# Kernel optimization log

Measured on AMD Instinct MI355X. Metric: run time of the kernel, lower is better.

Reference implementation:

```python
import jax, jax.numpy as jnp
import numpy as np

KH, KW = 3, 3
STRIDE, PAD, DIL = 1, 1, 1
GROUPS, DG = 1, 1
B, C, H, W = 4, 64, 96, 96
O = 64
K = KH * KW


def setup_inputs() -> dict:
    key = jax.random.key(0)
    k1, k2, k3, k4 = jax.random.split(key, 4)
    x = jax.random.normal(k1, (B, C, H, W), dtype=jnp.float32)
    offset = jax.random.normal(k2, (B, DG * 2 * K, H, W), dtype=jnp.float32)
    mask = jax.random.uniform(k3, (B, DG * K, H, W), dtype=jnp.float32)
    stdv = 1.0 / np.sqrt(C * KH * KW)
    weight = jax.random.uniform(k4, (O, C // GROUPS, KH, KW), dtype=jnp.float32,
                                minval=-stdv, maxval=stdv)
    bias = jnp.zeros((O,), dtype=jnp.float32)
    return {"x": x, "offset": offset, "mask": mask, "weight": weight, "bias": bias}


def _dcn(x, offset, mask, weight, bias):
    Bc, Cc, Hc, Wc = x.shape
    Ho = (Hc + 2 * PAD - DIL * (KH - 1) - 1) // STRIDE + 1
    Wo = (Wc + 2 * PAD - DIL * (KW - 1) - 1) // STRIDE + 1
    Cg = Cc // DG
    dt = x.dtype

    # offset channels per deform group: [k, (y,x)] interleaved (mmcv layout)
    off = offset.reshape(Bc, DG, K, 2, Ho, Wo)
    off_y, off_x = off[:, :, :, 0], off[:, :, :, 1]          # [B,DG,K,Ho,Wo]
    m = mask.reshape(Bc, DG, K, Ho, Wo)

    ky = (jnp.arange(K) // KW).astype(dt) * DIL               # kernel tap dy
    kx = (jnp.arange(K) % KW).astype(dt) * DIL                # kernel tap dx
    base_y = (jnp.arange(Ho) * STRIDE - PAD).astype(dt)
    base_x = (jnp.arange(Wo) * STRIDE - PAD).astype(dt)
    py = base_y[None, None, None, :, None] + ky[None, None, :, None, None] + off_y
    px = base_x[None, None, None, None, :] + kx[None, None, :, None, None] + off_x

    y0 = jnp.floor(py)
    x0 = jnp.floor(px)
    ly = py - y0
    lx = px - x0
    y0i = y0.astype(jnp.int32)
    x0i = x0.astype(jnp.int32)

    x_flat = x.reshape(Bc, DG, Cg, Hc * Wc)

    def gather(yi, xi):
        # zero-padding semantics: out-of-range corners contribute 0
        valid = ((yi >= 0) & (yi < Hc) & (xi >= 0) & (xi < Wc)).astype(dt)
        idx = jnp.clip(yi, 0, Hc - 1) * Wc + jnp.clip(xi, 0, Wc - 1)
        idx_b = jnp.broadcast_to(idx.reshape(Bc, DG, 1, K * Ho * Wo),
                                 (Bc, DG, Cg, K * Ho * Wo))
        vals = jnp.take_along_axis(x_flat, idx_b, axis=3)
        return vals.reshape(Bc, DG, Cg, K, Ho, Wo), valid

    v00, m00 = gather(y0i, x0i)
    v01, m01 = gather(y0i, x0i + 1)
    v10, m10 = gather(y0i + 1, x0i)
    v11, m11 = gather(y0i + 1, x0i + 1)

    w00 = ((1 - ly) * (1 - lx) * m00)[:, :, None]             # [B,DG,1,K,Ho,Wo]
    w01 = ((1 - ly) * lx * m01)[:, :, None]
    w10 = (ly * (1 - lx) * m10)[:, :, None]
    w11 = (ly * lx * m11)[:, :, None]

    sampled = v00 * w00 + v01 * w01 + v10 * w10 + v11 * w11   # bilinear
    sampled = sampled * m[:, :, None]                         # mask modulation
    s = sampled.reshape(Bc, Cc, K, Ho, Wo)

    out = jnp.einsum('ock,bckhw->bohw', weight.reshape(O, Cc, K), s)
    return out + bias[None, :, None, None]


def reference(x, offset, mask, weight, bias):
    return _dcn(x, offset, mask, weight, bias)
```

## Files before the change

### kernel.cpp

```cpp
#include <hip/hip_runtime.h>

#define Bn 4
#define Cn 64
#define Hn 96
#define Wn 96
#define On 64
#define Kn 9
#define HWn (Hn*Wn)
#define NT 256
#define TP 16
#define TW (Wn/TP)
#define NBLK (Bn*Hn*TW)
#define SSTRIDE 584
#define NWELEM (18*4*64*8)

typedef __attribute__((ext_vector_type(8))) short bf16x8;
typedef __attribute__((ext_vector_type(4))) short bf16x4;
typedef __attribute__((ext_vector_type(4))) float f32x4;

__device__ __forceinline__ unsigned short f2bf(float f) {
    unsigned u = __float_as_uint(f);
    u += 0x7FFFu + ((u >> 16) & 1u);
    return (unsigned short)(u >> 16);
}
__device__ __forceinline__ float bf2f(unsigned short h) {
    return __uint_as_float((unsigned)h << 16);
}
__device__ __forceinline__ unsigned cvtpk(float a, float b) {
    return (unsigned)f2bf(a) | ((unsigned)f2bf(b) << 16);
}

__global__ __launch_bounds__(NT) void prep_kernel(
    const float* __restrict__ x, const float* __restrict__ w,
    unsigned short* __restrict__ xT, unsigned short* __restrict__ wbfA)
{
    __shared__ unsigned short tile[Cn * Wn];
    const int tid = threadIdx.x;
    if (blockIdx.x < Bn * Hn) {
        const int b = blockIdx.x / Hn;
        const int h = blockIdx.x - b * Hn;
        #pragma unroll
        for (int i = 0; i < (Cn * Wn) / NT; ++i) {
            int e = i * NT + tid;
            int c = e / Wn, ww = e - c * Wn;
            tile[c * Wn + ww] = f2bf(x[(((size_t)b * Cn + c) * Hn + h) * Wn + ww]);
        }
        __syncthreads();
        #pragma unroll
        for (int i = 0; i < (Wn * 8) / NT; ++i) {
            int s = i * NT + tid;
            int ww = s >> 3, g = s & 7;
            unsigned short hh[8];
            #pragma unroll
            for (int j = 0; j < 8; ++j) hh[j] = tile[(g * 8 + j) * Wn + ww];
            uint4 pk;
            pk.x = hh[0] | ((unsigned)hh[1] << 16);
            pk.y = hh[2] | ((unsigned)hh[3] << 16);
            pk.z = hh[4] | ((unsigned)hh[5] << 16);
            pk.w = hh[6] | ((unsigned)hh[7] << 16);
            *(uint4*)&xT[(((size_t)b * Hn + h) * Wn + ww) * Cn + g * 8] = pk;
        }
    } else {
        int i = (blockIdx.x - Bn * Hn) * NT + tid;
        if (i < NWELEM) {
            int j  = i & 7;
            int l  = (i >> 3) & 63;
            int wv = (i >> 9) & 3;
            int t  = i >> 11;
            int o  = wv * 16 + (l & 15);
            int kp = t * 32 + (l >> 4) * 8 + j;
            wbfA[i] = f2bf(w[(o * Cn + (kp & 63)) * Kn + (kp >> 6)]);
        }
    }
}

__global__ __launch_bounds__(NT, 4) void dcn5_kernel(
    const unsigned short* __restrict__ xT, const float* __restrict__ offset,
    const float* __restrict__ mask, const float* __restrict__ bias,
    const unsigned short* __restrict__ wbfA, float* __restrict__ out)
{
    __shared__ float4 lwv[4][36];
    __shared__ int4   liv[4][36];
    __shared__ __align__(16) unsigned short Slds[TP * SSTRIDE];

    const int tid  = threadIdx.x;
    const int wave = tid >> 6;
    const int lane = tid & 63;

    const int p = blockIdx.x;
    const int v = (p & 7) * (NBLK / 8) + (p >> 3);
    const int b  = v / (Hn * TW);
    int rem      = v - b * (Hn * TW);
    const int ho = rem / TW;
    const int wt = rem - ho * TW;
    const int wo0 = wt * TP;

    const bf16x8* Af = (const bf16x8*)wbfA;
    bf16x8 aReg[3];
    aReg[0] = Af[(0 * 4 + wave) * 64 + lane];
    aReg[1] = Af[(1 * 4 + wave) * 64 + lane];
    aReg[2] = Af[(2 * 4 + wave) * 64 + lane];

    if (lane < 36) {
        int k  = lane >> 2;
        int pl = lane & 3;
        int wo = wo0 + wave * 4 + pl;
        float oy = offset[((b * (2*Kn) + 2*k    ) * Hn + ho) * Wn + wo];
        float ox = offset[((b * (2*Kn) + 2*k + 1) * Hn + ho) * Wn + wo];
        float mm = mask  [((b * Kn + k) * Hn + ho) * Wn + wo];
        float py = (float)(ho - 1 + (k / 3)) + oy;
        float px = (float)(wo - 1 + (k % 3)) + ox;
        float y0f = floorf(py), x0f = floorf(px);
        float ly = py - y0f, lx = px - x0f;
        int y0 = (int)y0f, x0i = (int)x0f;
        int y1 = y0 + 1,   x1i = x0i + 1;
        float vy0 = (y0  >= 0 && y0  < Hn) ? 1.f : 0.f;
        float vy1 = (y1  >= 0 && y1  < Hn) ? 1.f : 0.f;
        float vx0 = (x0i >= 0 && x0i < Wn) ? 1.f : 0.f;
        float vx1 = (x1i >= 0 && x1i < Wn) ? 1.f : 0.f;
        int cy0 = min(max(y0, 0),  Hn-1), cy1 = min(max(y1, 0),  Hn-1);
        int cx0 = min(max(x0i, 0), Wn-1), cx1 = min(max(x1i, 0), Wn-1);
        float4 wv;
        wv.x = (1.f - ly) * (1.f - lx) * mm * vy0 * vx0;
        wv.y = (1.f - ly) * lx         * mm * vy0 * vx1;
        wv.z = ly         * (1.f - lx) * mm * vy1 * vx0;
        wv.w = ly         * lx         * mm * vy1 * vx1;
        lwv[wave][lane] = wv;
        liv[wave][lane] = make_int4(cy0 * Wn + cx0, cy0 * Wn + cx1,
                                    cy1 * Wn + cx0, cy1 * Wn + cx1);
    }

    {
        const int pl  = lane >> 4;
        const int q   = lane & 15;
        const int gpx = wave * 4 + pl;
        const unsigned short* xb = xT + (size_t)b * HWn * Cn + q * 4;
        #pragma unroll
        for (int k = 0; k < Kn; ++k) {
            float4 wv = lwv[wave][k * 4 + pl];
            int4   iv = liv[wave][k * 4 + pl];
            bf16x4 v0 = *(const bf16x4*)(xb + ((size_t)iv.x << 6));
            bf16x4 v1 = *(const bf16x4*)(xb + ((size_t)iv.y << 6));
            bf16x4 v2 = *(const bf16x4*)(xb + ((size_t)iv.z << 6));
            bf16x4 v3 = *(const bf16x4*)(xb + ((size_t)iv.w << 6));
            float f[4];
            #pragma unroll
            for (int j = 0; j < 4; ++j) {
                f[j] = wv.x * bf2f((unsigned short)v0[j]) + wv.y * bf2f((unsigned short)v1[j])
                     + wv.z * bf2f((unsigned short)v2[j]) + wv.w * bf2f((unsigned short)v3[j]);
            }
            uint2 pk;
            pk.x = cvtpk(f[0], f[1]);
            pk.y = cvtpk(f[2], f[3]);
            *(uint2*)&Slds[gpx * SSTRIDE + k * 64 + q * 4] = pk;
        }
    }
    __syncthreads();

    const int n    = lane & 15;
    const int quad = lane >> 4;
    f32x4 acc = {0.f, 0.f, 0.f, 0.f};
    #pragma unroll
    for (int t = 0; t < 18; ++t) {
        bf16x8 aUse = aReg[t % 3];
        if (t + 3 < 18) aReg[t % 3] = Af[((t + 3) * 4 + wave) * 64 + lane];
        bf16x8 bf = *(const bf16x8*)&Slds[n * SSTRIDE + t * 32 + quad * 8];
        acc = __builtin_amdgcn_mfma_f32_16x16x32_bf16(aUse, bf, acc, 0, 0, 0);
    }

    #pragma unroll
    for (int r = 0; r < 4; ++r) {
        int o = wave * 16 + quad * 4 + r;
        out[(((size_t)b * On + o) * Hn + ho) * Wn + wo0 + n] = acc[r] + bias[o];
    }
}

__global__ __launch_bounds__(NT) void dcn_fallback_kernel(
    const float* __restrict__ x, const float* __restrict__ offset,
    const float* __restrict__ mask, const float* __restrict__ weight,
    const float* __restrict__ bias, float* __restrict__ out)
{
    int idx = blockIdx.x * NT + threadIdx.x;
    if (idx >= Bn * On * HWn) return;
    int wo = idx % Wn;
    int ho = (idx / Wn) % Hn;
    int o  = (idx / HWn) % On;
    int b  = idx / (On * HWn);
    float s = bias[o];
    for (int k = 0; k < Kn; ++k) {
        float oy = offset[((b * (2*Kn) + 2*k    ) * Hn + ho) * Wn + wo];
        float ox = offset[((b * (2*Kn) + 2*k + 1) * Hn + ho) * Wn + wo];
        float mm = mask  [((b * Kn + k) * Hn + ho) * Wn + wo];
        float py = (float)(ho - 1 + (k / 3)) + oy;
        float px = (float)(wo - 1 + (k % 3)) + ox;
        float y0f = floorf(py), x0f = floorf(px);
        float ly = py - y0f, lx = px - x0f;
        int y0 = (int)y0f, x0i = (int)x0f, y1 = y0 + 1, x1i = x0i + 1;
        float vy0 = (y0  >= 0 && y0  < Hn) ? 1.f : 0.f;
        float vy1 = (y1  >= 0 && y1  < Hn) ? 1.f : 0.f;
        float vx0 = (x0i >= 0 && x0i < Wn) ? 1.f : 0.f;
        float vx1 = (x1i >= 0 && x1i < Wn) ? 1.f : 0.f;
        int cy0 = min(max(y0, 0),  Hn-1), cy1 = min(max(y1, 0),  Hn-1);
        int cx0 = min(max(x0i, 0), Wn-1), cx1 = min(max(x1i, 0), Wn-1);
        float w0 = (1.f-ly)*(1.f-lx)*mm*vy0*vx0, w1 = (1.f-ly)*lx*mm*vy0*vx1;
        float w2 = ly*(1.f-lx)*mm*vy1*vx0,       w3 = ly*lx*mm*vy1*vx1;
        int i0 = cy0*Wn+cx0, i1 = cy0*Wn+cx1, i2 = cy1*Wn+cx0, i3 = cy1*Wn+cx1;
        for (int c = 0; c < Cn; ++c) {
            const float* xp = x + ((size_t)b * Cn + c) * HWn;
            float vv = w0*xp[i0] + w1*xp[i1] + w2*xp[i2] + w3*xp[i3];
            s += vv * weight[(o * Cn + c) * Kn + k];
        }
    }
    out[idx] = s;
}

extern "C" void kernel_launch(void* const* d_in, const int* in_sizes, int n_in,
                              void* d_out, int out_size, void* d_ws, size_t ws_size,
                              hipStream_t stream) {
    const float* x      = (const float*)d_in[0];
    const float* offset = (const float*)d_in[1];
    const float* mask   = (const float*)d_in[2];
    const float* weight = (const float*)d_in[3];
    const float* bias   = (const float*)d_in[4];
    float* out = (float*)d_out;

    const size_t xt_bytes = (size_t)Bn * HWn * Cn * sizeof(unsigned short);
    const size_t w_bytes  = (size_t)NWELEM * sizeof(unsigned short);

    if (ws_size >= xt_bytes + w_bytes) {
        unsigned short* xT   = (unsigned short*)d_ws;
        unsigned short* wbfA = (unsigned short*)((char*)d_ws + xt_bytes);
        prep_kernel<<<Bn * Hn + (NWELEM + NT - 1) / NT, NT, 0, stream>>>(x, weight, xT, wbfA);
        dcn5_kernel<<<NBLK, NT, 0, stream>>>(xT, offset, mask, bias, wbfA, out);
    } else {
        dcn_fallback_kernel<<<(Bn * On * HWn + NT - 1) / NT, NT, 0, stream>>>(
            x, offset, mask, weight, bias, out);
    }
}
```

Before: 90.81 us.

## Fuse bf16 prep into the DCN kernel using a per-tile LDS input window

Removes the separate prep kernel and its bf16 NHWC workspace. For each 16-pixel tile, the kernel stages a 9x24 halo window of all channels from fp32 NCHW input into LDS as bf16, and does bilinear sampling from that window. Samples that land outside the window fall back to direct fp32 global gathers. Weights are converted from fp32 into MFMA fragments held in registers, and each block now processes three tiles in a loop. The trade-off is that every tile reloads a large overlapping window, and the sample buffer is written with scattered 2-byte LDS stores, which costs extra L2 traffic and LDS bandwidth.

```diff
diff --git a/kernel.cpp b/kernel.cpp
--- a/kernel.cpp
+++ b/kernel.cpp
@@ -10,13 +10,20 @@
 #define NT 256
 #define TP 16
 #define TW (Wn/TP)
-#define NBLK (Bn*Hn*TW)
+#define TG 3
+#define NGRP (TW/TG)
+#define NBLK (Bn*Hn*NGRP)
+#define WR 9
+#define WC 24
+#define XSTR 72
+#define NPIX (WR*WC)
 #define SSTRIDE 584
-#define NWELEM (18*4*64*8)
+#define NKT 18
 
 typedef __attribute__((ext_vector_type(8))) short bf16x8;
 typedef __attribute__((ext_vector_type(4))) short bf16x4;
 typedef __attribute__((ext_vector_type(4))) float f32x4;
+typedef __attribute__((ext_vector_type(4))) unsigned u32x4;
 
 __device__ __forceinline__ unsigned short f2bf(float f) {
     unsigned u = __float_as_uint(f);
@@ -30,58 +37,15 @@
     return (unsigned)f2bf(a) | ((unsigned)f2bf(b) << 16);
 }
 
-__global__ __launch_bounds__(NT) void prep_kernel(
-    const float* __restrict__ x, const float* __restrict__ w,
-    unsigned short* __restrict__ xT, unsigned short* __restrict__ wbfA)
+__global__ __launch_bounds__(NT, 3) void dcn_fused_kernel(
+    const float* __restrict__ x, const float* __restrict__ offset,
+    const float* __restrict__ mask, const float* __restrict__ w,
+    const float* __restrict__ bias, float* __restrict__ out)
 {
-    __shared__ unsigned short tile[Cn * Wn];
-    const int tid = threadIdx.x;
-    if (blockIdx.x < Bn * Hn) {
-        const int b = blockIdx.x / Hn;
-        const int h = blockIdx.x - b * Hn;
-        #pragma unroll
-        for (int i = 0; i < (Cn * Wn) / NT; ++i) {
-            int e = i * NT + tid;
-            int c = e / Wn, ww = e - c * Wn;
-            tile[c * Wn + ww] = f2bf(x[(((size_t)b * Cn + c) * Hn + h) * Wn + ww]);
-        }
-        __syncthreads();
-        #pragma unroll
-        for (int i = 0; i < (Wn * 8) / NT; ++i) {
-            int s = i * NT + tid;
-            int ww = s >> 3, g = s & 7;
-            unsigned short hh[8];
-            #pragma unroll
-            for (int j = 0; j < 8; ++j) hh[j] = tile[(g * 8 + j) * Wn + ww];
-            uint4 pk;
-            pk.x = hh[0] | ((unsigned)hh[1] << 16);
-            pk.y = hh[2] | ((unsigned)hh[3] << 16);
-            pk.z = hh[4] | ((unsigned)hh[5] << 16);
-            pk.w = hh[6] | ((unsigned)hh[7] << 16);
-            *(uint4*)&xT[(((size_t)b * Hn + h) * Wn + ww) * Cn + g * 8] = pk;
-        }
-    } else {
-        int i = (blockIdx.x - Bn * Hn) * NT + tid;
-        if (i < NWELEM) {
-            int j  = i & 7;
-            int l  = (i >> 3) & 63;
-            int wv = (i >> 9) & 3;
-            int t  = i >> 11;
-            int o  = wv * 16 + (l & 15);
-            int kp = t * 32 + (l >> 4) * 8 + j;
-            wbfA[i] = f2bf(w[(o * Cn + (kp & 63)) * Kn + (kp >> 6)]);
-        }
-    }
-}
-
-__global__ __launch_bounds__(NT, 4) void dcn5_kernel(
-    const unsigned short* __restrict__ xT, const float* __restrict__ offset,
-    const float* __restrict__ mask, const float* __restrict__ bias,
-    const unsigned short* __restrict__ wbfA, float* __restrict__ out)
-{
+    __shared__ __align__(16) unsigned short xwin[NPIX * XSTR];
+    __shared__ __align__(16) unsigned short Slds[TP * SSTRIDE];
     __shared__ float4 lwv[4][36];
-    __shared__ int4   liv[4][36];
-    __shared__ __align__(16) unsigned short Slds[TP * SSTRIDE];
+    __shared__ int    lbs[4][36];
 
     const int tid  = threadIdx.x;
     const int wave = tid >> 6;
@@ -89,151 +53,160 @@
 
     const int p = blockIdx.x;
     const int v = (p & 7) * (NBLK / 8) + (p >> 3);
-    const int b  = v / (Hn * TW);
-    int rem      = v - b * (Hn * TW);
-    const int ho = rem / TW;
-    const int wt = rem - ho * TW;
-    const int wo0 = wt * TP;
-
-    const bf16x8* Af = (const bf16x8*)wbfA;
-    bf16x8 aReg[3];
-    aReg[0] = Af[(0 * 4 + wave) * 64 + lane];
-    aReg[1] = Af[(1 * 4 + wave) * 64 + lane];
-    aReg[2] = Af[(2 * 4 + wave) * 64 + lane];
-
-    if (lane < 36) {
-        int k  = lane >> 2;
-        int pl = lane & 3;
-        int wo = wo0 + wave * 4 + pl;
-        float oy = offset[((b * (2*Kn) + 2*k    ) * Hn + ho) * Wn + wo];
-        float ox = offset[((b * (2*Kn) + 2*k + 1) * Hn + ho) * Wn + wo];
-        float mm = mask  [((b * Kn + k) * Hn + ho) * Wn + wo];
-        float py = (float)(ho - 1 + (k / 3)) + oy;
-        float px = (float)(wo - 1 + (k % 3)) + ox;
-        float y0f = floorf(py), x0f = floorf(px);
-        float ly = py - y0f, lx = px - x0f;
-        int y0 = (int)y0f, x0i = (int)x0f;
-        int y1 = y0 + 1,   x1i = x0i + 1;
-        float vy0 = (y0  >= 0 && y0  < Hn) ? 1.f : 0.f;
-        float vy1 = (y1  >= 0 && y1  < Hn) ? 1.f : 0.f;
-        float vx0 = (x0i >= 0 && x0i < Wn) ? 1.f : 0.f;
-        float vx1 = (x1i >= 0 && x1i < Wn) ? 1.f : 0.f;
-        int cy0 = min(max(y0, 0),  Hn-1), cy1 = min(max(y1, 0),  Hn-1);
-        int cx0 = min(max(x0i, 0), Wn-1), cx1 = min(max(x1i, 0), Wn-1);
-        float4 wv;
-        wv.x = (1.f - ly) * (1.f - lx) * mm * vy0 * vx0;
-        wv.y = (1.f - ly) * lx         * mm * vy0 * vx1;
-        wv.z = ly         * (1.f - lx) * mm * vy1 * vx0;
-        wv.w = ly         * lx         * mm * vy1 * vx1;
-        lwv[wave][lane] = wv;
-        liv[wave][lane] = make_int4(cy0 * Wn + cx0, cy0 * Wn + cx1,
-                                    cy1 * Wn + cx0, cy1 * Wn + cx1);
+    const int b   = v / (Hn * NGRP);
+    int rem       = v - b * (Hn * NGRP);
+    const int ho  = rem / NGRP;
+    const int grp = rem - ho * NGRP;
+    const int wr0 = ho - 4;
+
+    bf16x8 afrag[NKT];
+    {
+        const float* wrow = w + ((wave * 16 + (lane & 15)) * (Cn * Kn))
+                              + ((lane >> 4) * 8);
+        #pragma unroll
+        for (int t = 0; t < NKT; ++t) {
+            float4 fa = *(const float4*)(wrow + t * 32);
+            float4 fb = *(const float4*)(wrow + t * 32 + 4);
+            u32x4 u;
+            u.x = cvtpk(fa.x, fa.y);
+            u.y = cvtpk(fa.z, fa.w);
+            u.z = cvtpk(fb.x, fb.y);
+            u.w = cvtpk(fb.z, fb.w);
+            afrag[t] = __builtin_bit_cast(bf16x8, u);
+        }
     }
 
-    {
-        const int pl  = lane >> 4;
-        const int q   = lane & 15;
-        const int gpx = wave * 4 + pl;
-        const unsigned short* xb = xT + (size_t)b * HWn * Cn + q * 4;
-        #pragma unroll
-        for (int k = 0; k < Kn; ++k) {
-            float4 wv = lwv[wave][k * 4 + pl];
-            int4   iv = liv[wave][k * 4 + pl];
-            bf16x4 v0 = *(const bf16x4*)(xb + ((size_t)iv.x << 6));
-            bf16x4 v1 = *(const bf16x4*)(xb + ((size_t)iv.y << 6));
-            bf16x4 v2 = *(const bf16x4*)(xb + ((size_t)iv.z << 6));
-            bf16x4 v3 = *(const bf16x4*)(xb + ((size_t)iv.w << 6));
-            float f[4];
+    for (int s = 0; s < TG; ++s) {
+        const int wt  = grp * TG + s;
+        const int wo0 = wt * TP;
+        const int wc0 = wo0 - 4;
+
+        {
+            const float* xb = x + (size_t)b * Cn * HWn;
+            #pragma unroll 4
+            for (int i = 0; i < (Cn / 2 * NPIX) / NT; ++i) {
+                int e   = i * NT + tid;
+                int cp  = e / NPIX;
+                int pix = e - cp * NPIX;
+                int r   = pix / WC;
+                int col = pix - r * WC;
+                int gr = wr0 + r, gc = wc0 + col;
+                bool ok = (gr >= 0) && (gr < Hn) && (gc >= 0) && (gc < Wn);
+                int cgr = min(max(gr, 0), Hn - 1);
+                int cgc = min(max(gc, 0), Wn - 1);
+                const float* src = xb + (size_t)(2 * cp) * HWn + cgr * Wn + cgc;
+                float v0 = src[0];
+                float v1 = src[HWn];
+                if (!ok) { v0 = 0.f; v1 = 0.f; }
+                *(unsigned*)&xwin[pix * XSTR + 2 * cp] = cvtpk(v0, v1);
+            }
+        }
+
+        if (lane < 36) {
+            const int k  = lane >> 2;
+            const int pl = lane & 3;
+            const int wo = wo0 + wave * 4 + pl;
+            float oy = offset[((b * (2*Kn) + 2*k    ) * Hn + ho) * Wn + wo];
+            float ox = offset[((b * (2*Kn) + 2*k + 1) * Hn + ho) * Wn + wo];
+            float mm = mask  [((b * Kn + k) * Hn + ho) * Wn + wo];
+            float py = (float)(ho - 1 + (k / 3)) + oy;
+            float px = (float)(wo - 1 + (k % 3)) + ox;
+            float y0f = floorf(py), x0f = floorf(px);
+            float ly = py - y0f, lx = px - x0f;
+            int y0 = (int)y0f, x0i = (int)x0f;
+            float vy0 = (y0     >= 0 && y0     < Hn) ? 1.f : 0.f;
+            float vy1 = (y0 + 1 >= 0 && y0 + 1 < Hn) ? 1.f : 0.f;
+            float vx0 = (x0i    >= 0 && x0i    < Wn) ? 1.f : 0.f;
+            float vx1 = (x0i+ 1 >= 0 && x0i+ 1 < Wn) ? 1.f : 0.f;
+            float4 wv;
+            wv.x = (1.f - ly) * (1.f - lx) * mm * vy0 * vx0;
+            wv.y = (1.f - ly) * lx         * mm * vy0 * vx1;
+            wv.z = ly         * (1.f - lx) * mm * vy1 * vx0;
+            wv.w = ly         * lx         * mm * vy1 * vx1;
+            lwv[wave][lane] = wv;
+            int ry = y0 - wr0, rx = x0i - wc0;
+            bool fast = (ry >= 0) && (ry <= WR - 2) && (rx >= 0) && (rx <= WC - 2);
+            lbs[wave][lane] = fast ? (ry * WC + rx) : -1;
+        }
+        __syncthreads();
+
+        {
+            const int pl  = lane >> 4;
+            const int q   = lane & 15;
+            const int gpx = wave * 4 + pl;
+            unsigned short* Srow = &Slds[gpx * SSTRIDE];
             #pragma unroll
-            for (int j = 0; j < 4; ++j) {
-                f[j] = wv.x * bf2f((unsigned short)v0[j]) + wv.y * bf2f((unsigned short)v1[j])
-                     + wv.z * bf2f((unsigned short)v2[j]) + wv.w * bf2f((unsigned short)v3[j]);
-            }
-            uint2 pk;
-            pk.x = cvtpk(f[0], f[1]);
-            pk.y = cvtpk(f[2], f[3]);
-            *(uint2*)&Slds[gpx * SSTRIDE + k * 64 + q * 4] = pk;
+            for (int k = 0; k < Kn; ++k) {
+                float4 wv = lwv[wave][k * 4 + pl];
+                int base  = lbs[wave][k * 4 + pl];
+                float f[4];
+                if (base >= 0) {
+                    const unsigned short* ppix = &xwin[base * XSTR + q * 4];
+                    bf16x4 v0 = *(const bf16x4*)(ppix);
+                    bf16x4 v1 = *(const bf16x4*)(ppix + XSTR);
+                    bf16x4 v2 = *(const bf16x4*)(ppix + WC * XSTR);
+                    bf16x4 v3 = *(const bf16x4*)(ppix + WC * XSTR + XSTR);
+                    #pragma unroll
+                    for (int j = 0; j < 4; ++j) {
+                        f[j] = wv.x * bf2f((unsigned short)v0[j])
+                             + wv.y * bf2f((unsigned short)v1[j])
+                             + wv.z * bf2f((unsigned short)v2[j])
+                             + wv.w * bf2f((unsigned short)v3[j]);
+                    }
+                } else {
+                    const int wo = wo0 + gpx;
+                    float oy = offset[((b * (2*Kn) + 2*k    ) * Hn + ho) * Wn + wo];
+                    float ox = offset[((b * (2*Kn) + 2*k + 1) * Hn + ho) * Wn + wo];
+                    float py = (float)(ho - 1 + (k / 3)) + oy;
+                    float px = (float)(wo - 1 + (k % 3)) + ox;
+                    int y0 = (int)floorf(py), x0i = (int)floorf(px);
+                    int cy0 = min(max(y0,     0), Hn - 1);
+                    int cy1 = min(max(y0 + 1, 0), Hn - 1);
+                    int cx0 = min(max(x0i,     0), Wn - 1);
+                    int cx1 = min(max(x0i + 1, 0), Wn - 1);
+                    int i00 = cy0 * Wn + cx0, i01 = cy0 * Wn + cx1;
+                    int i10 = cy1 * Wn + cx0, i11 = cy1 * Wn + cx1;
+                    const float* xc = x + ((size_t)b * Cn + q * 4) * HWn;
+                    #pragma unroll
+                    for (int j = 0; j < 4; ++j) {
+                        const float* xj = xc + (size_t)j * HWn;
+                        f[j] = wv.x * xj[i00] + wv.y * xj[i01]
+                             + wv.z * xj[i10] + wv.w * xj[i11];
+                    }
+                }
+                unsigned p01 = cvtpk(f[0], f[1]);
+                unsigned p23 = cvtpk(f[2], f[3]);
+                Srow[(q * 4 + 0) * Kn + k] = (unsigned short)(p01);
+                Srow[(q * 4 + 1) * Kn + k] = (unsigned short)(p01 >> 16);
+                Srow[(q * 4 + 2) * Kn + k] = (unsigned short)(p23);
+                Srow[(q * 4 + 3) * Kn + k] = (unsigned short)(p23 >> 16);
+            }
+        }
+        __syncthreads();
+
+        {
+            const int n    = lane & 15;
+            const int quad = lane >> 4;
+            f32x4 acc = {0.f, 0.f, 0.f, 0.f};
+            #pragma unroll
+            for (int t = 0; t < NKT; ++t) {
+                bf16x8 bFrag = *(const bf16x8*)&Slds[n * SSTRIDE + t * 32 + quad * 8];
+                acc = __builtin_amdgcn_mfma_f32_16x16x32_bf16(afrag[t], bFrag, acc, 0, 0, 0);
+            }
+            #pragma unroll
+            for (int r = 0; r < 4; ++r) {
+                int o = wave * 16 + quad * 4 + r;
+                out[(((size_t)b * On + o) * Hn + ho) * Wn + wo0 + n] = acc[r] + bias[o];
+            }
         }
     }
-    __syncthreads();
-
-    const int n    = lane & 15;
-    const int quad = lane >> 4;
-    f32x4 acc = {0.f, 0.f, 0.f, 0.f};
-    #pragma unroll
-    for (int t = 0; t < 18; ++t) {
-        bf16x8 aUse = aReg[t % 3];
-        if (t + 3 < 18) aReg[t % 3] = Af[((t + 3) * 4 + wave) * 64 + lane];
-        bf16x8 bf = *(const bf16x8*)&Slds[n * SSTRIDE + t * 32 + quad * 8];
-        acc = __builtin_amdgcn_mfma_f32_16x16x32_bf16(aUse, bf, acc, 0, 0, 0);
-    }
-
-    #pragma unroll
-    for (int r = 0; r < 4; ++r) {
-        int o = wave * 16 + quad * 4 + r;
-        out[(((size_t)b * On + o) * Hn + ho) * Wn + wo0 + n] = acc[r] + bias[o];
-    }
-}
-
-__global__ __launch_bounds__(NT) void dcn_fallback_kernel(
-    const float* __restrict__ x, const float* __restrict__ offset,
-    const float* __restrict__ mask, const float* __restrict__ weight,
-    const float* __restrict__ bias, float* __restrict__ out)
-{
-    int idx = blockIdx.x * NT + threadIdx.x;
-    if (idx >= Bn * On * HWn) return;
-    int wo = idx % Wn;
-    int ho = (idx / Wn) % Hn;
-    int o  = (idx / HWn) % On;
-    int b  = idx / (On * HWn);
-    float s = bias[o];
-    for (int k = 0; k < Kn; ++k) {
-        float oy = offset[((b * (2*Kn) + 2*k    ) * Hn + ho) * Wn + wo];
-        float ox = offset[((b * (2*Kn) + 2*k + 1) * Hn + ho) * Wn + wo];
-        float mm = mask  [((b * Kn + k) * Hn + ho) * Wn + wo];
-        float py = (float)(ho - 1 + (k / 3)) + oy;
-        float px = (float)(wo - 1 + (k % 3)) + ox;
-        float y0f = floorf(py), x0f = floorf(px);
-        float ly = py - y0f, lx = px - x0f;
-        int y0 = (int)y0f, x0i = (int)x0f, y1 = y0 + 1, x1i = x0i + 1;
-        float vy0 = (y0  >= 0 && y0  < Hn) ? 1.f : 0.f;
-        float vy1 = (y1  >= 0 && y1  < Hn) ? 1.f : 0.f;
-        float vx0 = (x0i >= 0 && x0i < Wn) ? 1.f : 0.f;
-        float vx1 = (x1i >= 0 && x1i < Wn) ? 1.f : 0.f;
-        int cy0 = min(max(y0, 0),  Hn-1), cy1 = min(max(y1, 0),  Hn-1);
-        int cx0 = min(max(x0i, 0), Wn-1), cx1 = min(max(x1i, 0), Wn-1);
-        float w0 = (1.f-ly)*(1.f-lx)*mm*vy0*vx0, w1 = (1.f-ly)*lx*mm*vy0*vx1;
-        float w2 = ly*(1.f-lx)*mm*vy1*vx0,       w3 = ly*lx*mm*vy1*vx1;
-        int i0 = cy0*Wn+cx0, i1 = cy0*Wn+cx1, i2 = cy1*Wn+cx0, i3 = cy1*Wn+cx1;
-        for (int c = 0; c < Cn; ++c) {
-            const float* xp = x + ((size_t)b * Cn + c) * HWn;
-            float vv = w0*xp[i0] + w1*xp[i1] + w2*xp[i2] + w3*xp[i3];
-            s += vv * weight[(o * Cn + c) * Kn + k];
-        }
-    }
-    out[idx] = s;
 }
 
 extern "C" void kernel_launch(void* const* d_in, const int* in_sizes, int n_in,
                               void* d_out, int out_size, void* d_ws, size_t ws_size,
                               hipStream_t stream) {
-    const float* x      = (const float*)d_in[0];
-    const float* offset = (const float*)d_in[1];
-    const float* mask   = (const float*)d_in[2];
-    const float* weight = (const float*)d_in[3];
-    const float* bias   = (const float*)d_in[4];
-    float* out = (float*)d_out;
-
-    const size_t xt_bytes = (size_t)Bn * HWn * Cn * sizeof(unsigned short);
-    const size_t w_bytes  = (size_t)NWELEM * sizeof(unsigned short);
-
-    if (ws_size >= xt_bytes + w_bytes) {
-        unsigned short* xT   = (unsigned short*)d_ws;
-        unsigned short* wbfA = (unsigned short*)((char*)d_ws + xt_bytes);
-        prep_kernel<<<Bn * Hn + (NWELEM + NT - 1) / NT, NT, 0, stream>>>(x, weight, xT, wbfA);
-        dcn5_kernel<<<NBLK, NT, 0, stream>>>(xT, offset, mask, bias, wbfA, out);
-    } else {
-        dcn_fallback_kernel<<<(Bn * On * HWn + NT - 1) / NT, NT, 0, stream>>>(
-            x, offset, mask, weight, bias, out);
-    }
-}
+    (void)in_sizes; (void)n_in; (void)out_size; (void)d_ws; (void)ws_size;
+    dcn_fused_kernel<<<NBLK, NT, 0, stream>>>(
+        (const float*)d_in[0], (const float*)d_in[1], (const float*)d_in[2],
+        (const float*)d_in[3], (const float*)d_in[4], (float*)d_out);
+}
```

Result: slower. 109.5 us (+20.5%).
